# Optimization experiments

Hardware: AMD Instinct MI355X
Metric: run time of the kernel (lower is better)

Reference implementation:

```python
import math
import jax, jax.numpy as jnp
import numpy as np

SEQ, BATCH, D_MODEL, HEADS = 2048, 2, 1024, 16
D_K = D_MODEL // HEADS


def setup_inputs() -> dict:
    key = jax.random.key(0)
    ks = jax.random.split(key, 11)
    s = 1.0 / math.sqrt(D_MODEL)
    inp = {
        "q": jax.random.normal(ks[0], (SEQ, BATCH, D_MODEL), jnp.float32),
        "k": jax.random.normal(ks[1], (SEQ, BATCH, D_MODEL), jnp.float32),
        "v": jax.random.normal(ks[2], (SEQ, BATCH, D_MODEL), jnp.float32),
        "Wq": jax.random.normal(ks[3], (D_MODEL, D_MODEL), jnp.float32) * s,
        "bq": jnp.zeros((D_MODEL,), jnp.float32),
        "Wk": jax.random.normal(ks[4], (D_MODEL, D_MODEL), jnp.float32) * s,
        "bk": jnp.zeros((D_MODEL,), jnp.float32),
        "Wv": jax.random.normal(ks[5], (D_MODEL, D_MODEL), jnp.float32) * s,
        "bv": jnp.zeros((D_MODEL,), jnp.float32),
        "Wo": jax.random.normal(ks[6], (D_MODEL, D_MODEL), jnp.float32) * s,
        "bo": jnp.zeros((D_MODEL,), jnp.float32),
    }
    return inp


def _proj(x, W, b):
    # [S,B,D] @ [D, H*Dk] -> [S,B,H,Dk]
    y = jnp.einsum('sbd,de->sbe', x, W) + b
    return y.reshape(x.shape[0], x.shape[1], HEADS, D_K)


def reference(q, k, v, Wq, bq, Wk, bk, Wv, bv, Wo, bo):
    scale = 1.0 / math.sqrt(D_K)
    query = _proj(q, Wq, bq)            # [i,b,h,d]
    key_ = _proj(k, Wk, bk)             # [j,b,h,d]
    value = _proj(v, Wv, bv)            # [j,b,h,d]
    scores = jnp.einsum('ibhd,jbhd->ijbh', query, key_) * scale
    attn = jax.nn.softmax(scores, axis=1)  # softmax over key axis j (dim=1)
    x = jnp.einsum('ijbh,jbhd->ibhd', attn, value)
    x = x.reshape(SEQ, BATCH, D_MODEL)
    return jnp.einsum('sbd,de->sbe', x, Wo) + bo
```

## Files before the change

kernel.cpp:

```cpp
#include <hip/hip_runtime.h>
#include <hip/hip_bf16.h>


typedef __attribute__((ext_vector_type(8))) short bf16x8;
typedef __attribute__((ext_vector_type(4))) float f32x4;

constexpr int SEQ   = 2048;
constexpr int BATCH = 2;
constexpr int DM    = 1024;
constexpr int DK    = 64;
constexpr int MR    = SEQ * BATCH;
constexpr int SST   = BATCH * DM;
constexpr int HD    = SEQ * DK;

__device__ __forceinline__ unsigned pkbf(float a, float b) {
    __hip_bfloat162 h = __float22bfloat162_rn(float2{a, b});
    union { __hip_bfloat162 h2; unsigned u; } cv;
    cv.h2 = h;
    return cv.u;
}

__device__ __forceinline__ f32x4 mfma16(bf16x8 a, bf16x8 b, f32x4 c) {
    return __builtin_amdgcn_mfma_f32_16x16x32_bf16(a, b, c, 0, 0, 0);
}

__device__ __forceinline__ void gl16(const unsigned short* g, unsigned short* l) {
    __builtin_amdgcn_global_load_lds(
        (const __attribute__((address_space(1))) void*)g,
        (__attribute__((address_space(3))) void*)l, 16, 0, 0);
}

__global__ __launch_bounds__(256)
void wt_prep_all(const float* __restrict__ w0, const float* __restrict__ w1,
                 const float* __restrict__ w2, const float* __restrict__ w3,
                 unsigned short* __restrict__ o0, unsigned short* __restrict__ o1,
                 unsigned short* __restrict__ o2, unsigned short* __restrict__ o3)
{
    const int z = blockIdx.z;
    const float* W = (z == 0) ? w0 : (z == 1) ? w1 : (z == 2) ? w2 : w3;
    unsigned short* Wt = (z == 0) ? o0 : (z == 1) ? o1 : (z == 2) ? o2 : o3;

    const int t = threadIdx.x;
    const int e = blockIdx.x * 64 + (t & 63);
    const int dq = blockIdx.y * 256 + (t >> 6) * 64;
    unsigned short* orow = Wt + (size_t)e * DM + dq;
#pragma unroll
    for (int c = 0; c < 8; ++c) {
        float f[8];
#pragma unroll
        for (int j = 0; j < 8; ++j)
            f[j] = W[(size_t)(dq + c * 8 + j) * DM + e];
        uint4 u = { pkbf(f[0], f[1]), pkbf(f[2], f[3]),
                    pkbf(f[4], f[5]), pkbf(f[6], f[7]) };
        *(uint4*)(orow + c * 8) = u;
    }
}

__global__ __launch_bounds__(256)
void qkv_cast(const float* __restrict__ qa, const float* __restrict__ ka,
              const float* __restrict__ va,
              unsigned short* __restrict__ Qb, unsigned short* __restrict__ Kb,
              unsigned short* __restrict__ Vb)
{
    const int z = blockIdx.y;
    const float* src = (z == 0) ? qa : (z == 1) ? ka : va;
    unsigned short* dst = (z == 0) ? Qb : (z == 1) ? Kb : Vb;
    const size_t i = ((size_t)blockIdx.x * 256 + threadIdx.x) * 8;
    float4 f0 = *(const float4*)(src + i);
    float4 f1 = *(const float4*)(src + i + 4);
    uint4 u = { pkbf(f0.x, f0.y), pkbf(f0.z, f0.w),
                pkbf(f1.x, f1.y), pkbf(f1.z, f1.w) };
    *(uint4*)(dst + i) = u;
}

__global__ __launch_bounds__(256)
void gemm_qkv_b(const unsigned short* __restrict__ Qb,
                const unsigned short* __restrict__ Kb,
                const unsigned short* __restrict__ Vb,
                const unsigned short* __restrict__ wq,
                const unsigned short* __restrict__ wk,
                const unsigned short* __restrict__ wv,
                const float* __restrict__ bq, const float* __restrict__ bk,
                const float* __restrict__ bv,
                unsigned short* __restrict__ Qh, unsigned short* __restrict__ Kh,
                unsigned short* __restrict__ Vtp)
{
    constexpr int K = 1024;
    __shared__ unsigned short As[128 * 32];
    __shared__ unsigned short Bs[128 * 32];

    const int z = blockIdx.z;
    const unsigned short* Ab = (z == 0) ? Qb : (z == 1) ? Kb : Vb;
    const unsigned short* Bt = (z == 0) ? wq : (z == 1) ? wk : wv;
    const float* bias = (z == 0) ? bq : (z == 1) ? bk : bv;

    const int l = blockIdx.x + 8 * blockIdx.y;
    const int xcd = l & 7, jj0 = l >> 3;
    const int bm = xcd * 4 + (jj0 >> 3);
    const int bn = jj0 & 7;

    const int tid = threadIdx.x;
    const int wave = tid >> 6, lane = tid & 63;
    const int wr = wave >> 1, wc = wave & 1;
    const int lrow = lane & 15, g = lane >> 4;
    const int gr = lane & 15, gc = (lane >> 4) * 8;

    f32x4 acc[4][4] = {};

    for (int k0 = 0; k0 < K; k0 += 32) {
        gl16(Ab + (size_t)(bm * 128 + wave * 32 + gr) * K + k0 + gc,
             As + (2 * wave) * 512);
        gl16(Ab + (size_t)(bm * 128 + wave * 32 + 16 + gr) * K + k0 + gc,
             As + (2 * wave + 1) * 512);
        gl16(Bt + (size_t)(bn * 128 + wave * 32 + gr) * K + k0 + gc,
             Bs + (2 * wave) * 512);
        gl16(Bt + (size_t)(bn * 128 + wave * 32 + 16 + gr) * K + k0 + gc,
             Bs + (2 * wave + 1) * 512);
        __syncthreads();

        bf16x8 af[4], bfr[4];
#pragma unroll
        for (int i = 0; i < 4; ++i)
            af[i] = *(const bf16x8*)&As[(wr * 4 + i) * 512 + lane * 8];
#pragma unroll
        for (int j = 0; j < 4; ++j)
            bfr[j] = *(const bf16x8*)&Bs[(wc * 4 + j) * 512 + lane * 8];
#pragma unroll
        for (int i = 0; i < 4; ++i)
#pragma unroll
            for (int j = 0; j < 4; ++j)
                acc[i][j] = mfma16(af[i], bfr[j], acc[i][j]);
        __syncthreads();
    }

#pragma unroll
    for (int j = 0; j < 4; ++j) {
        const int col = bn * 128 + wc * 64 + j * 16 + lrow;
        const float bb = bias[col];
        const int h = col >> 6, d = col & 63;
#pragma unroll
        for (int i = 0; i < 4; ++i) {
            const int row0 = bm * 128 + wr * 64 + i * 16 + 4 * g;
#pragma unroll
            for (int r = 0; r < 4; ++r) {
                const float v = acc[i][j][r] + bb;
                const unsigned short bfv = (unsigned short)(pkbf(v, v) & 0xffffu);
                const int row = row0 + r;
                const int s = row >> 1, b = row & 1;
                if (z != 2) {
                    unsigned short* C = (z == 0) ? Qh : Kh;
                    C[(size_t)(b * 16 + h) * HD + s * 64 + d] = bfv;
                } else {
                    const int st = s >> 6, sl = s & 63;
                    const int kc = sl >> 5, r5 = sl & 31;
                    const int h2 = r5 >> 4, gg = (r5 >> 2) & 3, jv = r5 & 3;
                    const int sp = kc * 32 + gg * 8 + h2 * 4 + jv;
                    Vtp[(size_t)(b * 16 + h) * HD + (size_t)d * SEQ + st * 64 + sp] = bfv;
                }
            }
        }
    }
}

__global__ __launch_bounds__(256)
void attn_mfma(const unsigned short* __restrict__ Qh,
               const unsigned short* __restrict__ Kh,
               const unsigned short* __restrict__ Vtp,
               unsigned short* __restrict__ Xp)
{
    __shared__ unsigned short lds[16384];

    const int tid = threadIdx.x;
    const int fid = blockIdx.x;
    const int xcd = fid & 7, idx = fid >> 3;
    const int bh = xcd * 4 + (idx >> 4);
    const int qt = idx & 15;

    const int wave = tid >> 6, lane = tid & 63;
    const int lrow = lane & 15, g = lane >> 4;
    const int s7 = lrow & 7;
    const int q0w = qt * 128 + wave * 32;
    const float CE = 0.18033688011112042592f;

    const unsigned short* qb = Qh + (size_t)bh * HD;
    const unsigned short* kb = Kh + (size_t)bh * HD;
    const unsigned short* vb = Vtp + (size_t)bh * HD;

    unsigned short* K0 = lds;
    unsigned short* V0 = lds + 4096;
    unsigned short* K1 = lds + 8192;
    unsigned short* V1 = lds + 12288;

    const int r8 = lane >> 3, c8 = lane & 7;
    const unsigned short* ksrcA = kb + (size_t)(wave * 16 + r8) * 64 + (c8 ^ r8) * 8;
    const unsigned short* ksrcB = ksrcA + 8 * 64;
    const unsigned short* vsrcA = vb + (size_t)(wave * 16 + r8) * SEQ + (c8 ^ r8) * 8;
    const unsigned short* vsrcB = vsrcA + 8 * SEQ;

    auto stage = [&](unsigned short* kbuf, unsigned short* vbuf, int t) {
        const size_t ko = (size_t)t * 4096;
        const size_t vo = (size_t)t * 64;
        gl16(ksrcA + ko, kbuf + wave * 1024);
        gl16(ksrcB + ko, kbuf + wave * 1024 + 512);
        gl16(vsrcA + vo, vbuf + wave * 1024);
        gl16(vsrcB + vo, vbuf + wave * 1024 + 512);
    };

    bf16x8 bq[2][2];
#pragma unroll
    for (int qi = 0; qi < 2; ++qi)
#pragma unroll
        for (int dc = 0; dc < 2; ++dc)
            bq[qi][dc] = *(const bf16x8*)(qb + (size_t)(q0w + qi * 16 + lrow) * 64
                                             + dc * 32 + g * 8);

    f32x4 oacc[4][2] = {};
    float lsum0 = 0.f, lsum1 = 0.f;

    const int off0 = lrow * 64 + ((g ^ s7) * 8);
    const int off1 = lrow * 64 + (((4 + g) ^ s7) * 8);

    auto compute = [&](const unsigned short* kbuf, const unsigned short* vbuf) {
        bf16x8 ak[4][2];
#pragma unroll
        for (int kt = 0; kt < 4; ++kt) {
            ak[kt][0] = *(const bf16x8*)(kbuf + kt * 1024 + off0);
            ak[kt][1] = *(const bf16x8*)(kbuf + kt * 1024 + off1);
        }

        uint4 pbu[2][2];
#pragma unroll
        for (int qi = 0; qi < 2; ++qi) {
            float ll = 0.f;
#pragma unroll
            for (int kt = 0; kt < 4; ++kt) {
                f32x4 s = { 0.f, 0.f, 0.f, 0.f };
                s = mfma16(ak[kt][0], bq[qi][0], s);
                s = mfma16(ak[kt][1], bq[qi][1], s);
                const float p0 = __builtin_amdgcn_exp2f(s[0] * CE);
                const float p1 = __builtin_amdgcn_exp2f(s[1] * CE);
                const float p2 = __builtin_amdgcn_exp2f(s[2] * CE);
                const float p3 = __builtin_amdgcn_exp2f(s[3] * CE);
                ll += (p0 + p1) + (p2 + p3);
                const unsigned lo = pkbf(p0, p1);
                const unsigned hi = pkbf(p2, p3);
                if (kt & 1) { pbu[kt >> 1][qi].z = lo; pbu[kt >> 1][qi].w = hi; }
                else        { pbu[kt >> 1][qi].x = lo; pbu[kt >> 1][qi].y = hi; }
            }
            if (qi == 0) lsum0 += ll; else lsum1 += ll;
        }

        bf16x8 av[4][2];
#pragma unroll
        for (int dt = 0; dt < 4; ++dt) {
            av[dt][0] = *(const bf16x8*)(vbuf + dt * 1024 + off0);
            av[dt][1] = *(const bf16x8*)(vbuf + dt * 1024 + off1);
        }

        __builtin_amdgcn_s_setprio(1);
#pragma unroll
        for (int kc = 0; kc < 2; ++kc)
#pragma unroll
            for (int dt = 0; dt < 4; ++dt)
#pragma unroll
                for (int qi = 0; qi < 2; ++qi) {
                    union { uint4 u; bf16x8 v; } cv;
                    cv.u = pbu[kc][qi];
                    oacc[dt][qi] = mfma16(av[dt][kc], cv.v, oacc[dt][qi]);
                }
        __builtin_amdgcn_s_setprio(0);
    };

    stage(K0, V0, 0);
    asm volatile("s_waitcnt vmcnt(0)" ::: "memory");
    __syncthreads();

#pragma unroll 1
    for (int tt = 0; tt < 16; ++tt) {
        stage(K1, V1, 2 * tt + 1);
        compute(K0, V0);
        __syncthreads();
        if (tt < 15) stage(K0, V0, 2 * tt + 2);
        compute(K1, V1);
        __syncthreads();
    }

    float l0 = lsum0; l0 += __shfl_xor(l0, 16); l0 += __shfl_xor(l0, 32);
    float l1 = lsum1; l1 += __shfl_xor(l1, 16); l1 += __shfl_xor(l1, 32);
    const float inv0 = 1.0f / l0, inv1 = 1.0f / l1;

    unsigned short (*osh)[72] = (unsigned short (*)[72])(lds + wave * 32 * 72);
#pragma unroll
    for (int qi = 0; qi < 2; ++qi) {
        const float inv = qi ? inv1 : inv0;
#pragma unroll
        for (int dt = 0; dt < 4; ++dt) {
            const int d0 = dt * 16 + 4 * g;
            const unsigned u0 = pkbf(oacc[dt][qi][0] * inv, oacc[dt][qi][1] * inv);
            const unsigned u1 = pkbf(oacc[dt][qi][2] * inv, oacc[dt][qi][3] * inv);
            *(unsigned*)&osh[qi * 16 + lrow][d0] = u0;
            *(unsigned*)&osh[qi * 16 + lrow][d0 + 2] = u1;
        }
    }
    const int ql = lane >> 1;
    const int dh = (lane & 1) * 32;
    unsigned short* xrow = Xp + (size_t)(q0w + ql) * SST + bh * 64 + dh;
#pragma unroll
    for (int c = 0; c < 4; ++c) {
        uint4 vv = *(const uint4*)&osh[ql][dh + c * 8];
        *(uint4*)(xrow + c * 8) = vv;
    }
}

__global__ __launch_bounds__(256)
void gemm_out(const unsigned short* __restrict__ Xp,
              const unsigned short* __restrict__ WtO,
              const float* __restrict__ bias, float* __restrict__ out)
{
    constexpr int K = 1024, N = 1024;
    __shared__ unsigned short As[128 * 32];
    __shared__ unsigned short Bs[64 * 32];

    const int l = blockIdx.x + 16 * blockIdx.y;
    const int xcd = l & 7, jj0 = l >> 3;
    const int bm = xcd * 4 + (jj0 >> 4);
    const int bn = jj0 & 15;

    const int tid = threadIdx.x;
    const int wave = tid >> 6, lane = tid & 63;
    const int wr = wave >> 1, wc = wave & 1;
    const int lrow = lane & 15, g = lane >> 4;
    const int gr = lane & 15, gc = (lane >> 4) * 8;

    f32x4 acc[4][2] = {};

    for (int k0 = 0; k0 < K; k0 += 32) {
        gl16(Xp + (size_t)(bm * 128 + wave * 32 + gr) * K + k0 + gc,
             As + (2 * wave) * 512);
        gl16(Xp + (size_t)(bm * 128 + wave * 32 + 16 + gr) * K + k0 + gc,
             As + (2 * wave + 1) * 512);
        gl16(WtO + (size_t)(bn * 64 + wave * 16 + gr) * K + k0 + gc,
             Bs + wave * 512);
        __syncthreads();

        bf16x8 af[4], bfr[2];
#pragma unroll
        for (int i = 0; i < 4; ++i)
            af[i] = *(const bf16x8*)&As[(wr * 4 + i) * 512 + lane * 8];
#pragma unroll
        for (int j = 0; j < 2; ++j)
            bfr[j] = *(const bf16x8*)&Bs[(wc * 2 + j) * 512 + lane * 8];
#pragma unroll
        for (int i = 0; i < 4; ++i)
#pragma unroll
            for (int j = 0; j < 2; ++j)
                acc[i][j] = mfma16(af[i], bfr[j], acc[i][j]);
        __syncthreads();
    }

#pragma unroll
    for (int j = 0; j < 2; ++j) {
        const int col = bn * 64 + wc * 32 + j * 16 + lrow;
        const float bb = bias[col];
#pragma unroll
        for (int i = 0; i < 4; ++i) {
            const int row0 = bm * 128 + wr * 64 + i * 16 + 4 * g;
#pragma unroll
            for (int r = 0; r < 4; ++r)
                out[(size_t)(row0 + r) * N + col] = acc[i][j][r] + bb;
        }
    }
}

extern "C" void kernel_launch(void* const* d_in, const int* in_sizes, int n_in,
                              void* d_out, int out_size, void* d_ws, size_t ws_size,
                              hipStream_t stream) {
    (void)in_sizes; (void)n_in; (void)out_size; (void)ws_size;

    const float* q  = (const float*)d_in[0];
    const float* k  = (const float*)d_in[1];
    const float* v  = (const float*)d_in[2];
    const float* Wq = (const float*)d_in[3];
    const float* bq = (const float*)d_in[4];
    const float* Wk = (const float*)d_in[5];
    const float* bk = (const float*)d_in[6];
    const float* Wv = (const float*)d_in[7];
    const float* bv = (const float*)d_in[8];
    const float* Wo = (const float*)d_in[9];
    const float* bo = (const float*)d_in[10];
    float* out = (float*)d_out;

    unsigned short* ws = (unsigned short*)d_ws;
    const size_t WSZ = (size_t)DM * DM;
    const size_t MSZ = (size_t)MR * DM;
    unsigned short* WtQ = ws;
    unsigned short* WtK = ws + WSZ;
    unsigned short* WtV = ws + 2 * WSZ;
    unsigned short* WtO = ws + 3 * WSZ;
    unsigned short* Qb  = ws + 4 * WSZ;
    unsigned short* Kb  = Qb + MSZ;
    unsigned short* Vb  = Kb + MSZ;
    unsigned short* Qh  = Vb + MSZ;
    unsigned short* Kh  = Qh + MSZ;
    unsigned short* Vtp = Kh + MSZ;
    unsigned short* Xp  = Vtp + MSZ;

    const dim3 blk(256);

    wt_prep_all<<<dim3(16, 4, 4), blk, 0, stream>>>(Wq, Wk, Wv, Wo, WtQ, WtK, WtV, WtO);

    qkv_cast<<<dim3(2048, 3), blk, 0, stream>>>(q, k, v, Qb, Kb, Vb);

    gemm_qkv_b<<<dim3(8, 32, 3), blk, 0, stream>>>(Qb, Kb, Vb, WtQ, WtK, WtV,
                                                   bq, bk, bv, Qh, Kh, Vtp);

    attn_mfma<<<dim3(512), blk, 0, stream>>>(Qh, Kh, Vtp, Xp);

    gemm_out<<<dim3(16, 32), blk, 0, stream>>>(Xp, WtO, bo, out);
}
```

Baseline: 154.0 us.

## Double-buffer LDS tiles in QKV and output projection GEMMs

Both projection GEMMs now use two LDS buffers per operand. Each step issues the global-to-LDS loads for the next K-slab before running the MFMAs on the current one, with a two-step loop and a prologue load, so memory latency overlaps compute instead of serialising on a barrier every iteration. Wave priority is raised with s_setprio around the MFMA block. The cost is twice the LDS footprint per block, which may reduce occupancy. Correctness relies on __syncthreads also waiting for the outstanding async LDS loads.

```diff
diff --git a/kernel.cpp b/kernel.cpp
--- a/kernel.cpp
+++ b/kernel.cpp
@@ -86,8 +86,8 @@
                 unsigned short* __restrict__ Vtp)
 {
     constexpr int K = 1024;
-    __shared__ unsigned short As[128 * 32];
-    __shared__ unsigned short Bs[128 * 32];
+    __shared__ unsigned short As[2][128 * 32];
+    __shared__ unsigned short Bs[2][128 * 32];
 
     const int z = blockIdx.z;
     const unsigned short* Ab = (z == 0) ? Qb : (z == 1) ? Kb : Vb;
@@ -105,31 +105,53 @@
     const int lrow = lane & 15, g = lane >> 4;
     const int gr = lane & 15, gc = (lane >> 4) * 8;
 
+    const unsigned short* aRow0 = Ab + (size_t)(bm * 128 + wave * 32 + gr) * K + gc;
+    const unsigned short* aRow1 = aRow0 + (size_t)16 * K;
+    const unsigned short* bRow0 = Bt + (size_t)(bn * 128 + wave * 32 + gr) * K + gc;
+    const unsigned short* bRow1 = bRow0 + (size_t)16 * K;
+
     f32x4 acc[4][4] = {};
 
-    for (int k0 = 0; k0 < K; k0 += 32) {
-        gl16(Ab + (size_t)(bm * 128 + wave * 32 + gr) * K + k0 + gc,
-             As + (2 * wave) * 512);
-        gl16(Ab + (size_t)(bm * 128 + wave * 32 + 16 + gr) * K + k0 + gc,
-             As + (2 * wave + 1) * 512);
-        gl16(Bt + (size_t)(bn * 128 + wave * 32 + gr) * K + k0 + gc,
-             Bs + (2 * wave) * 512);
-        gl16(Bt + (size_t)(bn * 128 + wave * 32 + 16 + gr) * K + k0 + gc,
-             Bs + (2 * wave + 1) * 512);
-        __syncthreads();
-
+    auto stageA = [&](int k0) {
+        gl16(aRow0 + k0, As[0] + (2 * wave) * 512);
+        gl16(aRow1 + k0, As[0] + (2 * wave + 1) * 512);
+        gl16(bRow0 + k0, Bs[0] + (2 * wave) * 512);
+        gl16(bRow1 + k0, Bs[0] + (2 * wave + 1) * 512);
+    };
+    auto stageB = [&](int k0) {
+        gl16(aRow0 + k0, As[1] + (2 * wave) * 512);
+        gl16(aRow1 + k0, As[1] + (2 * wave + 1) * 512);
+        gl16(bRow0 + k0, Bs[1] + (2 * wave) * 512);
+        gl16(bRow1 + k0, Bs[1] + (2 * wave + 1) * 512);
+    };
+    auto compute = [&](const unsigned short* as, const unsigned short* bs) {
         bf16x8 af[4], bfr[4];
 #pragma unroll
         for (int i = 0; i < 4; ++i)
-            af[i] = *(const bf16x8*)&As[(wr * 4 + i) * 512 + lane * 8];
+            af[i] = *(const bf16x8*)&as[(wr * 4 + i) * 512 + lane * 8];
 #pragma unroll
         for (int j = 0; j < 4; ++j)
-            bfr[j] = *(const bf16x8*)&Bs[(wc * 4 + j) * 512 + lane * 8];
+            bfr[j] = *(const bf16x8*)&bs[(wc * 4 + j) * 512 + lane * 8];
+        __builtin_amdgcn_s_setprio(1);
 #pragma unroll
         for (int i = 0; i < 4; ++i)
 #pragma unroll
             for (int j = 0; j < 4; ++j)
                 acc[i][j] = mfma16(af[i], bfr[j], acc[i][j]);
+        __builtin_amdgcn_s_setprio(0);
+    };
+
+    stageA(0);
+    asm volatile("s_waitcnt vmcnt(0)" ::: "memory");
+    __syncthreads();
+
+#pragma unroll 1
+    for (int k0 = 0; k0 < K; k0 += 64) {
+        stageB(k0 + 32);
+        compute(As[0], Bs[0]);
+        __syncthreads();
+        if (k0 + 64 < K) stageA(k0 + 64);
+        compute(As[1], Bs[1]);
         __syncthreads();
     }
 
@@ -318,8 +340,8 @@
               const float* __restrict__ bias, float* __restrict__ out)
 {
     constexpr int K = 1024, N = 1024;
-    __shared__ unsigned short As[128 * 32];
-    __shared__ unsigned short Bs[64 * 32];
+    __shared__ unsigned short As[2][128 * 32];
+    __shared__ unsigned short Bs[2][64 * 32];
 
     const int l = blockIdx.x + 16 * blockIdx.y;
     const int xcd = l & 7, jj0 = l >> 3;
@@ -332,29 +354,50 @@
     const int lrow = lane & 15, g = lane >> 4;
     const int gr = lane & 15, gc = (lane >> 4) * 8;
 
+    const unsigned short* aRow0 = Xp + (size_t)(bm * 128 + wave * 32 + gr) * K + gc;
+    const unsigned short* aRow1 = aRow0 + (size_t)16 * K;
+    const unsigned short* bRow0 = WtO + (size_t)(bn * 64 + wave * 16 + gr) * K + gc;
+
     f32x4 acc[4][2] = {};
 
-    for (int k0 = 0; k0 < K; k0 += 32) {
-        gl16(Xp + (size_t)(bm * 128 + wave * 32 + gr) * K + k0 + gc,
-             As + (2 * wave) * 512);
-        gl16(Xp + (size_t)(bm * 128 + wave * 32 + 16 + gr) * K + k0 + gc,
-             As + (2 * wave + 1) * 512);
-        gl16(WtO + (size_t)(bn * 64 + wave * 16 + gr) * K + k0 + gc,
-             Bs + wave * 512);
-        __syncthreads();
-
+    auto stageA = [&](int k0) {
+        gl16(aRow0 + k0, As[0] + (2 * wave) * 512);
+        gl16(aRow1 + k0, As[0] + (2 * wave + 1) * 512);
+        gl16(bRow0 + k0, Bs[0] + wave * 512);
+    };
+    auto stageB = [&](int k0) {
+        gl16(aRow0 + k0, As[1] + (2 * wave) * 512);
+        gl16(aRow1 + k0, As[1] + (2 * wave + 1) * 512);
+        gl16(bRow0 + k0, Bs[1] + wave * 512);
+    };
+    auto compute = [&](const unsigned short* as, const unsigned short* bs) {
         bf16x8 af[4], bfr[2];
 #pragma unroll
         for (int i = 0; i < 4; ++i)
-            af[i] = *(const bf16x8*)&As[(wr * 4 + i) * 512 + lane * 8];
+            af[i] = *(const bf16x8*)&as[(wr * 4 + i) * 512 + lane * 8];
 #pragma unroll
         for (int j = 0; j < 2; ++j)
-            bfr[j] = *(const bf16x8*)&Bs[(wc * 2 + j) * 512 + lane * 8];
+            bfr[j] = *(const bf16x8*)&bs[(wc * 2 + j) * 512 + lane * 8];
+        __builtin_amdgcn_s_setprio(1);
 #pragma unroll
         for (int i = 0; i < 4; ++i)
 #pragma unroll
             for (int j = 0; j < 2; ++j)
                 acc[i][j] = mfma16(af[i], bfr[j], acc[i][j]);
+        __builtin_amdgcn_s_setprio(0);
+    };
+
+    stageA(0);
+    asm volatile("s_waitcnt vmcnt(0)" ::: "memory");
+    __syncthreads();
+
+#pragma unroll 1
+    for (int k0 = 0; k0 < K; k0 += 64) {
+        stageB(k0 + 32);
+        compute(As[0], Bs[0]);
+        __syncthreads();
+        if (k0 + 64 < K) stageA(k0 + 64);
+        compute(As[1], Bs[1]);
         __syncthreads();
     }
 
```

Result: no change. 154.3 us (+0.2%).
